# Optimization experiments

Hardware: AMD Instinct MI355X
Metric: run time of the kernel (lower is better)

The kernel has to match this reference:

```python
import jax, jax.numpy as jnp
import numpy as np

B, Lq, Lk = 2, 4096, 1024
Q_DIM, KV_DIM = 2048, 2048
H, HD = 16, 128          # n_heads, head_dim (nope part)
KVC, QC, R = 512, 768, 64  # kv_comp_dim, q_comp_dim, retr_dim (RoPE part)
LOOKBACK = 8
NEG = -1e30


def setup_inputs() -> dict:
    key = jax.random.key(0)
    ks = jax.random.split(key, 11)
    def w(k, shape, fan_in):
        return jax.random.normal(k, shape, jnp.float32) / np.sqrt(fan_in).astype(np.float32)
    return {
        'q': jax.random.normal(ks[0], (B, Lq, Q_DIM), jnp.float32),
        'kv': jax.random.normal(ks[1], (B, Lk, KV_DIM), jnp.float32),
        'seg_id': jnp.sort(jax.random.randint(ks[2], (B, Lq), 0, Lk), axis=-1),
        'W_kvc': w(ks[3], (KV_DIM, KVC), KV_DIM),   # kv_comp linear (no bias)
        'W_dq':  w(ks[4], (Q_DIM, QC), Q_DIM),      # query down-projection
        'W_uq':  w(ks[5], (QC, H * HD), QC),        # query up-proj (nope)
        'W_qr':  w(ks[6], (QC, H * R), QC),         # query rope proj
        'W_uk':  w(ks[7], (KVC, H * HD), KVC),      # key up-proj (nope)
        'W_kr':  w(ks[8], (KVC, R), KVC),           # shared key rope proj
        'W_uv':  w(ks[9], (KVC, H * HD), KVC),      # value up-proj
        'W_o':   w(ks[10], (H * HD, Q_DIM), H * HD),# output projection
    }


def _rope(x, L):
    # x: [..., L, R] with R even; positions 0..L-1 on the -2 axis.
    half = x.shape[-1] // 2
    inv_freq = 1.0 / (10000.0 ** (jnp.arange(half, dtype=jnp.float32) / half))
    ang = jnp.arange(L, dtype=jnp.float32)[:, None] * inv_freq  # [L, half]
    cos, sin = jnp.cos(ang), jnp.sin(ang)
    x1, x2 = x[..., :half], x[..., half:]
    return jnp.concatenate([x1 * cos - x2 * sin, x1 * sin + x2 * cos], axis=-1)


def reference(q, kv, seg_id, W_kvc, W_dq, W_uq, W_qr, W_uk, W_kr, W_uv, W_o):
    b, lq, _ = q.shape
    lk = kv.shape[1]
    kv_c = kv @ W_kvc                                   # [B,Lk,KVC]
    q_c = q @ W_dq                                      # [B,Lq,QC]
    q_nope = (q_c @ W_uq).reshape(b, lq, H, HD).transpose(0, 2, 1, 3)  # [B,H,Lq,HD]
    q_rope = (q_c @ W_qr).reshape(b, lq, H, R).transpose(0, 2, 1, 3)   # [B,H,Lq,R]
    k_nope = (kv_c @ W_uk).reshape(b, lk, H, HD)        # [B,Lk,H,HD]
    v = (kv_c @ W_uv).reshape(b, lk, H, HD)             # [B,Lk,H,HD]
    k_rope = kv_c @ W_kr                                # [B,Lk,R] shared across heads
    q_rope = _rope(q_rope, lq)
    k_rope = _rope(k_rope, lk)
    scale = 1.0 / np.sqrt(HD + R).astype(np.float32)
    scores = (jnp.einsum('bhqd,bkhd->bhqk', q_nope, k_nope)
              + jnp.einsum('bhqr,bkr->bhqk', q_rope, k_rope)) * scale
    # segment lookback block mask: allow q_seg - lookback <= k <= q_seg
    k_ids = jnp.arange(lk)[None, None, :]               # [1,1,Lk]
    qs = seg_id[:, :, None]                             # [B,Lq,1]
    good = (k_ids <= qs) & (k_ids >= qs - LOOKBACK)     # [B,Lq,Lk]
    scores = jnp.where(good[:, None, :, :], scores, NEG)
    attn = jax.nn.softmax(scores, axis=-1)              # [B,H,Lq,Lk]
    out = jnp.einsum('bhqk,bkhd->bqhd', attn, v).reshape(b, lq, H * HD)
    return out @ W_o                                    # [B,Lq,Q_DIM]
```

## Files before the change

### kernel.cpp

```cpp
#include <hip/hip_runtime.h>
#include <math.h>

typedef __bf16 bf16_t;
typedef __bf16 bf16x8 __attribute__((ext_vector_type(8)));
typedef float f32x4 __attribute__((ext_vector_type(4)));

#define B_    2
#define LQ    4096
#define LK    1024
#define QDIM  2048
#define KVDIM 2048
#define H_    16
#define HD_   128
#define KVC_  512
#define QC_   768
#define R_    64

#define QCOMB 3072
#define KCOMB 4224

typedef __attribute__((address_space(1))) void gvoid_t;
typedef __attribute__((address_space(3))) void lvoid_t;

static __device__ __forceinline__ void gld_lds16(const void* g, void* l) {
  __builtin_amdgcn_global_load_lds((gvoid_t*)(void*)g, (lvoid_t*)l, 16, 0, 0);
}

__global__ void cvt2_f32_bf16(const float* __restrict__ a, bf16_t* __restrict__ oa, long na,
                              const float* __restrict__ b, bf16_t* __restrict__ ob, long nb) {
  const long stride = (long)gridDim.x * blockDim.x * 8;
  for (long i = ((long)blockIdx.x * blockDim.x + threadIdx.x) * 8; i < na; i += stride) {
    float4 x = *(const float4*)(a + i);
    float4 y = *(const float4*)(a + i + 4);
    bf16x8 t;
    t[0] = (bf16_t)x.x; t[1] = (bf16_t)x.y; t[2] = (bf16_t)x.z; t[3] = (bf16_t)x.w;
    t[4] = (bf16_t)y.x; t[5] = (bf16_t)y.y; t[6] = (bf16_t)y.z; t[7] = (bf16_t)y.w;
    *(bf16x8*)(oa + i) = t;
  }
  for (long i = ((long)blockIdx.x * blockDim.x + threadIdx.x) * 8; i < nb; i += stride) {
    float4 x = *(const float4*)(b + i);
    float4 y = *(const float4*)(b + i + 4);
    bf16x8 t;
    t[0] = (bf16_t)x.x; t[1] = (bf16_t)x.y; t[2] = (bf16_t)x.z; t[3] = (bf16_t)x.w;
    t[4] = (bf16_t)y.x; t[5] = (bf16_t)y.y; t[6] = (bf16_t)y.z; t[7] = (bf16_t)y.w;
    *(bf16x8*)(ob + i) = t;
  }
}

struct TransAll {
  const float* src[8];
  bf16_t* dst[8];
  int K[8], N[8], gx[8];
  int off[9];
};

__global__ __launch_bounds__(256) void transpose_all(TransAll d) {
  const int bid = blockIdx.x;
  int i = 0;
#pragma unroll
  for (int j = 1; j < 8; ++j) if (bid >= d.off[j]) i = j;
  const float* __restrict__ src = d.src[i];
  bf16_t* __restrict__ dst = d.dst[i];
  const int K = d.K[i], N = d.N[i];
  const int local = bid - d.off[i];
  const int gx = d.gx[i];
  const int bx = (local % gx) * 32, by = (local / gx) * 32;
  __shared__ float t[32][33];
  const int x = threadIdx.x, y = threadIdx.y;
#pragma unroll
  for (int j = 0; j < 32; j += 8)
    t[y + j][x] = src[(size_t)(by + y + j) * N + bx + x];
  __syncthreads();
#pragma unroll
  for (int j = 0; j < 32; j += 8)
    dst[(size_t)(bx + y + j) * K + by + x] = (bf16_t)t[x][y + j];
}

template <typename CT>
__global__ __launch_bounds__(256) void gemm_bt(
    const bf16_t* __restrict__ A, const bf16_t* __restrict__ Bt,
    CT* __restrict__ C, int M, int N, int K) {
  __shared__ __align__(16) bf16_t lA[128 * 64];
  __shared__ __align__(16) bf16_t lB[128 * 64];
  const int tid = threadIdx.x;
  const int wave = tid >> 6, lane = tid & 63;

  const int gx = gridDim.x, gy = gridDim.y;
  const int nwg = gx * gy;
  int bx, by;
  if (((nwg & 7) == 0) && ((gy & 7) == 0)) {
    const int orig = blockIdx.y * gx + blockIdx.x;
    const int wg = (orig & 7) * (nwg >> 3) + (orig >> 3);
    const int gxB = gx << 3;
    const int band = wg / gxB, rem = wg % gxB;
    bx = rem >> 3;
    by = (band << 3) + (rem & 7);
  } else {
    bx = blockIdx.x; by = blockIdx.y;
  }

  const int row0 = by * 128, col0 = bx * 128;
  const int wr = (wave >> 1) * 64, wc = (wave & 1) * 64;
  f32x4 acc[4][4] = {};
  const int kT = K >> 6;
  const int lr = lane >> 3;
  const int lc8 = (lane & 7) * 8;

  for (int kt = 0; kt < kT; ++kt) {
    const int k0 = kt << 6;
    __syncthreads();
#pragma unroll
    for (int j = 0; j < 4; ++j) {
      const int c = wave * 4 + j;
      const bf16_t* ga = A + (size_t)(row0 + c * 8 + lr) * K + k0 + lc8;
      gld_lds16(ga, &lA[c * 512]);
      const bf16_t* gb = Bt + (size_t)(col0 + c * 8 + lr) * K + k0 + lc8;
      gld_lds16(gb, &lB[c * 512]);
    }
    __syncthreads();
#pragma unroll
    for (int kk = 0; kk < 2; ++kk) {
      bf16x8 af[4], bfr[4];
      const int kc = kk * 32 + (lane >> 4) * 8;
      const int fr = lane & 15;
#pragma unroll
      for (int m = 0; m < 4; ++m)
        af[m] = *(const bf16x8*)&lA[(wr + m * 16 + fr) * 64 + kc];
#pragma unroll
      for (int n = 0; n < 4; ++n)
        bfr[n] = *(const bf16x8*)&lB[(wc + n * 16 + fr) * 64 + kc];
#pragma unroll
      for (int m = 0; m < 4; ++m)
#pragma unroll
        for (int n = 0; n < 4; ++n)
          acc[m][n] = __builtin_amdgcn_mfma_f32_16x16x32_bf16(af[m], bfr[n], acc[m][n], 0, 0, 0);
    }
  }
  const int fr = lane & 15, fq = lane >> 4;
#pragma unroll
  for (int m = 0; m < 4; ++m)
#pragma unroll
    for (int n = 0; n < 4; ++n) {
      const int col = col0 + wc + n * 16 + fr;
#pragma unroll
      for (int r = 0; r < 4; ++r) {
        const int row = row0 + wr + m * 16 + fq * 4 + r;
        C[(size_t)row * N + col] = (CT)acc[m][n][r];
      }
    }
}

template <int TN, typename CT>
__global__ __launch_bounds__(512, 2) void gemm_big2(
    const bf16_t* __restrict__ A, const bf16_t* __restrict__ Bt,
    CT* __restrict__ C, int M, int N, int K) {
  constexpr int NF = TN / 64;
  constexpr int LW = 4 + TN / 64;
  __shared__ __align__(16) bf16_t lA[2][256 * 64];
  __shared__ __align__(16) bf16_t lB[2][TN * 64];
  const int tid = threadIdx.x;
  const int w = tid >> 6, lane = tid & 63;

  const int gx = gridDim.x;
  const int nwg = gx * gridDim.y;
  const int orig = blockIdx.y * gx + blockIdx.x;
  const int wg = (orig & 7) * (nwg >> 3) + (orig >> 3);
  const int bx = wg % gx, by = wg / gx;

  const int row0 = by * 256, col0 = bx * TN;
  const int wm = w >> 2, wn = w & 3;
  const int lr = lane >> 3;
  const int kswz = ((lane & 7) ^ lr) * 8;
  const int nt = K >> 6;
  const int fr = lane & 15, fq = lane >> 4;

  auto STAGE = [&](int t, int buf) {
    const int k0 = t << 6;
#pragma unroll
    for (int j = 0; j < 4; ++j) {
      const int s = j * 8 + w;
      gld_lds16(A + (size_t)(row0 + s * 8 + lr) * K + k0 + kswz, &lA[buf][s * 512]);
    }
#pragma unroll
    for (int j = 0; j < TN / 64; ++j) {
      const int s = j * 8 + w;
      gld_lds16(Bt + (size_t)(col0 + s * 8 + lr) * K + k0 + kswz, &lB[buf][s * 512]);
    }
  };

  bf16x8 aA[8], bA[NF], aB[8], bB[NF];
  f32x4 acc[8][NF];
#pragma unroll
  for (int i = 0; i < 8; ++i)
#pragma unroll
    for (int j = 0; j < NF; ++j) acc[i][j] = f32x4{0.f, 0.f, 0.f, 0.f};

  auto READ = [&](int buf, int kk, bf16x8* a, bf16x8* b) {
    const int swzk = (kk * 32 + fq * 8) ^ ((fr & 7) << 3);
#pragma unroll
    for (int mf = 0; mf < 8; ++mf)
      a[mf] = *(const bf16x8*)&lA[buf][(wm * 128 + mf * 16 + fr) * 64 + swzk];
#pragma unroll
    for (int nf = 0; nf < NF; ++nf)
      b[nf] = *(const bf16x8*)&lB[buf][(wn * (TN / 4) + nf * 16 + fr) * 64 + swzk];
  };
  auto MF = [&](bf16x8* a, bf16x8* b) {
    __builtin_amdgcn_s_setprio(1);
#pragma unroll
    for (int mf = 0; mf < 8; ++mf)
#pragma unroll
      for (int nf = 0; nf < NF; ++nf)
        acc[mf][nf] = __builtin_amdgcn_mfma_f32_16x16x32_bf16(a[mf], b[nf], acc[mf][nf], 0, 0, 0);
    __builtin_amdgcn_s_setprio(0);
  };

  STAGE(0, 0);
  STAGE(1, 1);
  if constexpr (LW == 8) { asm volatile("s_waitcnt vmcnt(8)" ::: "memory"); }
  else                   { asm volatile("s_waitcnt vmcnt(6)" ::: "memory"); }
  __builtin_amdgcn_sched_barrier(0);
  __builtin_amdgcn_s_barrier();
  READ(0, 0, aA, bA);

  for (int t = 0; t < nt; ++t) {
    const int buf = t & 1;
    READ(buf, 1, aB, bB);
    __builtin_amdgcn_sched_barrier(0);
    MF(aA, bA);
    asm volatile("s_waitcnt lgkmcnt(0)" ::: "memory");
    __builtin_amdgcn_sched_barrier(0);
    __builtin_amdgcn_s_barrier();
    if (t + 2 < nt) {
      STAGE(t + 2, buf);
      if constexpr (LW == 8) { asm volatile("s_waitcnt vmcnt(8)" ::: "memory"); }
      else                   { asm volatile("s_waitcnt vmcnt(6)" ::: "memory"); }
    } else {
      asm volatile("s_waitcnt vmcnt(0)" ::: "memory");
    }
    __builtin_amdgcn_sched_barrier(0);
    __builtin_amdgcn_s_barrier();
    if (t + 1 < nt) READ(buf ^ 1, 0, aA, bA);
    __builtin_amdgcn_sched_barrier(0);
    MF(aB, bB);
  }

#pragma unroll
  for (int mf = 0; mf < 8; ++mf)
#pragma unroll
    for (int nf = 0; nf < NF; ++nf) {
      const int col = col0 + wn * (TN / 4) + nf * 16 + fr;
#pragma unroll
      for (int r = 0; r < 4; ++r) {
        const int row = row0 + wm * 128 + mf * 16 + fq * 4 + r;
        C[(size_t)row * N + col] = (CT)acc[mf][nf][r];
      }
    }
}

#define SWZK_(ks) (((ks) * 32 + fq * 8) ^ ((fr & 7) << 3))
#define RD_A(buf, q) { _Pragma("unroll") for (int mf = 0; mf < 4; ++mf) { \
    ar[mf][0] = *(const bf16x8*)&lA[buf][wm][((q) * 64 + mf * 16 + fr) * 64 + SWZK_(0)]; \
    ar[mf][1] = *(const bf16x8*)&lA[buf][wm][((q) * 64 + mf * 16 + fr) * 64 + SWZK_(1)]; } }
#define RD_B(buf, nq) { _Pragma("unroll") for (int nf = 0; nf < 2; ++nf) { \
    br[nq][nf][0] = *(const bf16x8*)&lB[buf][wbh][(wbr + (nq) * 32 + nf * 16 + fr) * 64 + SWZK_(0)]; \
    br[nq][nf][1] = *(const bf16x8*)&lB[buf][wbh][(wbr + (nq) * 32 + nf * 16 + fr) * 64 + SWZK_(1)]; } }
#define MFMA_Q(mq, nq) { __builtin_amdgcn_s_setprio(1); \
  _Pragma("unroll") for (int mf = 0; mf < 4; ++mf) \
  _Pragma("unroll") for (int nf = 0; nf < 2; ++nf) { \
    acc[(mq)*4+mf][(nq)*2+nf] = __builtin_amdgcn_mfma_f32_16x16x32_bf16(ar[mf][0], br[nq][nf][0], acc[(mq)*4+mf][(nq)*2+nf], 0, 0, 0); \
    acc[(mq)*4+mf][(nq)*2+nf] = __builtin_amdgcn_mfma_f32_16x16x32_bf16(ar[mf][1], br[nq][nf][1], acc[(mq)*4+mf][(nq)*2+nf], 0, 0, 0); } \
  __builtin_amdgcn_s_setprio(0); }
#define SBAR_ __builtin_amdgcn_sched_barrier(0)
#define HBAR_ __builtin_amdgcn_s_barrier()
#define LGK0_ asm volatile("s_waitcnt lgkmcnt(0)" ::: "memory")

template <typename CT>
__global__ __launch_bounds__(512, 2) void gemm_8ph(
    const bf16_t* __restrict__ A, const bf16_t* __restrict__ Bt,
    CT* __restrict__ C, int M, int N, int K) {
  __shared__ __align__(16) bf16_t lA[2][2][128 * 64];
  __shared__ __align__(16) bf16_t lB[2][2][128 * 64];
  const int tid = threadIdx.x;
  const int w = tid >> 6, lane = tid & 63;

  const int gx = gridDim.x;
  const int nwg = gx * gridDim.y;
  const int orig = blockIdx.y * gx + blockIdx.x;
  const int wg = (orig & 7) * (nwg >> 3) + (orig >> 3);
  const int bx = wg % gx, by = wg / gx;

  const int row0 = by * 256, col0 = bx * 256;
  const int wm = w >> 2, wn = w & 3;
  const int lr = lane >> 3;
  const int kswz = ((lane & 7) ^ lr) * 8;
  const int nt = K >> 6;
  const int fr = lane & 15, fq = lane >> 4;
  const int wbh = wn >> 1;
  const int wbr = (wn & 1) * 64;

  auto stA = [&](int t, int h, int buf) {
    const bf16_t* g = A + (size_t)(row0 + h * 128 + w * 8 + lr) * K + (t << 6) + kswz;
    gld_lds16(g, &lA[buf][h][w * 8 * 64]);
    gld_lds16(g + (size_t)64 * K, &lA[buf][h][(64 + w * 8) * 64]);
  };
  auto stB = [&](int t, int h, int buf) {
    const bf16_t* g = Bt + (size_t)(col0 + h * 128 + w * 8 + lr) * K + (t << 6) + kswz;
    gld_lds16(g, &lB[buf][h][w * 8 * 64]);
    gld_lds16(g + (size_t)64 * K, &lB[buf][h][(64 + w * 8) * 64]);
  };

  bf16x8 ar[4][2], br[2][2][2];
  f32x4 acc[8][4];
#pragma unroll
  for (int i = 0; i < 8; ++i)
#pragma unroll
    for (int j = 0; j < 4; ++j) acc[i][j] = f32x4{0.f, 0.f, 0.f, 0.f};

  stA(0, 0, 0); stA(0, 1, 0); stB(0, 0, 0); stB(0, 1, 0);
  stB(1, 0, 1); stB(1, 1, 1);
  asm volatile("s_waitcnt vmcnt(4)" ::: "memory");
  SBAR_; HBAR_;

  for (int t = 0; t < nt; ++t) {
    const int buf = t & 1;
    SBAR_;
    RD_A(buf, 0); RD_B(buf, 0);
    if (t + 1 < nt) stA(t + 1, 0, buf ^ 1);
    SBAR_; HBAR_; LGK0_; SBAR_;
    MFMA_Q(0, 0);
    SBAR_; HBAR_;
    SBAR_;
    RD_B(buf, 1);
    if (t + 1 < nt) stA(t + 1, 1, buf ^ 1);
    SBAR_; HBAR_; LGK0_; SBAR_;
    MFMA_Q(0, 1);
    SBAR_; HBAR_;
    SBAR_;
    RD_A(buf, 1);
    if (t + 2 < nt) stB(t + 2, 0, buf);
    SBAR_; HBAR_; LGK0_; SBAR_;
    MFMA_Q(1, 1);
    SBAR_; HBAR_;
    SBAR_;
    if (t + 2 < nt) {
      stB(t + 2, 1, buf);
      asm volatile("s_waitcnt vmcnt(4)" ::: "memory");
    } else {
      asm volatile("s_waitcnt vmcnt(0)" ::: "memory");
    }
    SBAR_; HBAR_; SBAR_;
    MFMA_Q(1, 0);
    SBAR_; HBAR_;
  }

#pragma unroll
  for (int mfg = 0; mfg < 8; ++mfg)
#pragma unroll
    for (int nfg = 0; nfg < 4; ++nfg) {
      const int col = col0 + wn * 64 + (nfg >> 1) * 32 + (nfg & 1) * 16 + fr;
#pragma unroll
      for (int r = 0; r < 4; ++r) {
        const int row = row0 + wm * 128 + mfg * 16 + fq * 4 + r;
        C[(size_t)row * N + col] = (CT)acc[mfg][nfg][r];
      }
    }
}

#define QROPE_BLOCKS ((B_ * LQ * H_) / 8)
__global__ __launch_bounds__(256) void rope2_kernel(bf16_t* __restrict__ qbase, bf16_t* __restrict__ kvbase) {
  const int bid = blockIdx.x;
  bf16_t* base;
  int tokStride, hshift, posMask;
  long bidl;
  if (bid < QROPE_BLOCKS) { base = qbase; tokStride = QCOMB; hshift = 4; posMask = LQ - 1; bidl = bid; }
  else { base = kvbase; tokStride = KCOMB; hshift = 0; posMask = LK - 1; bidl = bid - QROPE_BLOCKS; }
  const long idx = bidl * 8 + (threadIdx.x >> 5);
  const int i = threadIdx.x & 31;
  const long tok = idx >> hshift;
  const int h = (int)(idx & ((1 << hshift) - 1));
  const int pos = (int)(tok & posMask);
  bf16_t* p = base + tok * (long)tokStride + h * 64;
  const float x1 = (float)p[i], x2 = (float)p[i + 32];
  const float invf = expf(-((float)i * (1.0f / 32.f)) * 9.210340371976184f);
  float sn, cs;
  sincosf((float)pos * invf, &sn, &cs);
  p[i]      = (bf16_t)(x1 * cs - x2 * sn);
  p[i + 32] = (bf16_t)(x1 * sn + x2 * cs);
}

__global__ __launch_bounds__(256) void attn_sparse(
    const bf16_t* __restrict__ qc, const bf16_t* __restrict__ kvc,
    const int* __restrict__ seg, bf16_t* __restrict__ out) {
  const int qrow = blockIdx.x * 4 + (threadIdx.x >> 6);
  const int lane = threadIdx.x & 63;
  const int h = lane >> 2, sub = lane & 3;
  const int b = qrow >> 12;
  const int s = seg[qrow];
  const int kl = max(0, s - 8);
  const float scale = 0.07216878364870322f;

  float qnf[32], qrf[16];
  {
    const bf16_t* p = qc + (size_t)qrow * QCOMB + h * HD_ + sub * 32;
#pragma unroll
    for (int j = 0; j < 4; ++j) {
      bf16x8 t = *(const bf16x8*)(p + j * 8);
#pragma unroll
      for (int e = 0; e < 8; ++e) qnf[j * 8 + e] = (float)t[e];
    }
    const bf16_t* p2 = qc + (size_t)qrow * QCOMB + 2048 + h * R_ + sub * 16;
#pragma unroll
    for (int j = 0; j < 2; ++j) {
      bf16x8 t = *(const bf16x8*)(p2 + j * 8);
#pragma unroll
      for (int e = 0; e < 8; ++e) qrf[j * 8 + e] = (float)t[e];
    }
  }

  float sc[9];
#pragma unroll
  for (int kk = 0; kk < 9; ++kk) {
    const int kx = kl + kk;
    const bf16_t* kb = kvc + (size_t)(b * LK + kx) * KCOMB;
    float d = 0.f;
    const bf16_t* p = kb + h * HD_ + sub * 32;
#pragma unroll
    for (int j = 0; j < 4; ++j) {
      bf16x8 t = *(const bf16x8*)(p + j * 8);
#pragma unroll
      for (int e = 0; e < 8; ++e) d += qnf[j * 8 + e] * (float)t[e];
    }
    const bf16_t* p2 = kb + 4096 + sub * 16;
#pragma unroll
    for (int j = 0; j < 2; ++j) {
      bf16x8 t = *(const bf16x8*)(p2 + j * 8);
#pragma unroll
      for (int e = 0; e < 8; ++e) d += qrf[j * 8 + e] * (float)t[e];
    }
    d += __shfl_xor(d, 1);
    d += __shfl_xor(d, 2);
    sc[kk] = (kx <= s) ? d * scale : -1e30f;
  }
  float m = sc[0];
#pragma unroll
  for (int kk = 1; kk < 9; ++kk) m = fmaxf(m, sc[kk]);
  float sum = 0.f;
#pragma unroll
  for (int kk = 0; kk < 9; ++kk) { const float p = expf(sc[kk] - m); sc[kk] = p; sum += p; }
  const float inv = 1.f / sum;

  float o[32];
#pragma unroll
  for (int j = 0; j < 32; ++j) o[j] = 0.f;
#pragma unroll
  for (int kk = 0; kk < 9; ++kk) {
    const bf16_t* pv = kvc + (size_t)(b * LK + kl + kk) * KCOMB + 2048 + h * HD_ + sub * 32;
    const float p = sc[kk] * inv;
#pragma unroll
    for (int j = 0; j < 4; ++j) {
      bf16x8 t = *(const bf16x8*)(pv + j * 8);
#pragma unroll
      for (int e = 0; e < 8; ++e) o[j * 8 + e] += p * (float)t[e];
    }
  }
  bf16_t* po = out + (size_t)qrow * (H_ * HD_) + h * HD_ + sub * 32;
#pragma unroll
  for (int j = 0; j < 4; ++j) {
    bf16x8 t;
#pragma unroll
    for (int e = 0; e < 8; ++e) t[e] = (bf16_t)o[j * 8 + e];
    *(bf16x8*)(po + j * 8) = t;
  }
}

extern "C" void kernel_launch(void* const* d_in, const int* in_sizes, int n_in,
                              void* d_out, int out_size, void* d_ws, size_t ws_size,
                              hipStream_t stream) {
  const float* q     = (const float*)d_in[0];
  const float* kv    = (const float*)d_in[1];
  const int*   seg   = (const int*)d_in[2];
  const float* W_kvc = (const float*)d_in[3];
  const float* W_dq  = (const float*)d_in[4];
  const float* W_uq  = (const float*)d_in[5];
  const float* W_qr  = (const float*)d_in[6];
  const float* W_uk  = (const float*)d_in[7];
  const float* W_kr  = (const float*)d_in[8];
  const float* W_uv  = (const float*)d_in[9];
  const float* W_o   = (const float*)d_in[10];
  float* out = (float*)d_out;
  (void)in_sizes; (void)n_in; (void)out_size; (void)ws_size;

  char* ws = (char*)d_ws;
  size_t off = 0;
  auto alloc = [&](size_t bytes) {
    char* p = ws + off;
    off = (off + bytes + 255) & ~(size_t)255;
    return p;
  };
  bf16_t* q_bf    = (bf16_t*)alloc((size_t)B_ * LQ * QDIM * 2);
  bf16_t* kv_bf   = (bf16_t*)alloc((size_t)B_ * LK * KVDIM * 2);
  bf16_t* WkvcT   = (bf16_t*)alloc((size_t)KVC_ * KVDIM * 2);
  bf16_t* WdqT    = (bf16_t*)alloc((size_t)QC_ * QDIM * 2);
  bf16_t* WuqrT   = (bf16_t*)alloc((size_t)QCOMB * QC_ * 2);
  bf16_t* WkvT    = (bf16_t*)alloc((size_t)KCOMB * KVC_ * 2);
  bf16_t* WoT     = (bf16_t*)alloc((size_t)QDIM * (H_ * HD_) * 2);
  bf16_t* kv_c    = (bf16_t*)alloc((size_t)B_ * LK * KVC_ * 2);
  bf16_t* q_c     = (bf16_t*)alloc((size_t)B_ * LQ * QC_ * 2);
  bf16_t* q_comb  = (bf16_t*)alloc((size_t)B_ * LQ * QCOMB * 2);
  bf16_t* kv_comb = (bf16_t*)alloc((size_t)B_ * LK * KCOMB * 2);
  bf16_t* attn_o  = q_bf;

  cvt2_f32_bf16<<<4096, 256, 0, stream>>>(q, q_bf, (long)B_ * LQ * QDIM,
                                          kv, kv_bf, (long)B_ * LK * KVDIM);

  {
    TransAll d;
    auto set = [&](int i, const float* s, bf16_t* dt, int K, int N) {
      d.src[i] = s; d.dst[i] = dt; d.K[i] = K; d.N[i] = N; d.gx[i] = N / 32;
    };
    set(0, W_kvc, WkvcT, KVDIM, KVC_);
    set(1, W_dq,  WdqT,  QDIM,  QC_);
    set(2, W_uq,  WuqrT, QC_,   H_ * HD_);
    set(3, W_qr,  WuqrT + (size_t)(H_ * HD_) * QC_, QC_, H_ * R_);
    set(4, W_uk,  WkvT,  KVC_,  H_ * HD_);
    set(5, W_uv,  WkvT + (size_t)(H_ * HD_) * KVC_, KVC_, H_ * HD_);
    set(6, W_kr,  WkvT + (size_t)2 * (H_ * HD_) * KVC_, KVC_, R_);
    set(7, W_o,   WoT,   H_ * HD_, QDIM);
    int acc_off = 0;
    for (int i = 0; i < 8; ++i) {
      d.off[i] = acc_off;
      acc_off += (d.N[i] / 32) * (d.K[i] / 32);
    }
    d.off[8] = acc_off;
    transpose_all<<<acc_off, dim3(32, 8), 0, stream>>>(d);
  }

  gemm_bt<bf16_t><<<dim3(KVC_ / 128, (B_ * LK) / 128), 256, 0, stream>>>(
      kv_bf, WkvcT, kv_c, B_ * LK, KVC_, KVDIM);
  gemm_big2<128, bf16_t><<<dim3(QC_ / 128, (B_ * LQ) / 256), 512, 0, stream>>>(
      q_bf, WdqT, q_c, B_ * LQ, QC_, QDIM);
  gemm_8ph<bf16_t><<<dim3(QCOMB / 256, (B_ * LQ) / 256), 512, 0, stream>>>(
      q_c, WuqrT, q_comb, B_ * LQ, QCOMB, QC_);
  gemm_big2<128, bf16_t><<<dim3(KCOMB / 128, (B_ * LK) / 256), 512, 0, stream>>>(
      kv_c, WkvT, kv_comb, B_ * LK, KCOMB, KVC_);

  rope2_kernel<<<QROPE_BLOCKS + (B_ * LK) / 8, 256, 0, stream>>>(q_comb + 2048, kv_comb + 4096);

  attn_sparse<<<(B_ * LQ) / 4, 256, 0, stream>>>(q_comb, kv_comb, seg, attn_o);

  gemm_8ph<float><<<dim3(QDIM / 256, (B_ * LQ) / 256), 512, 0, stream>>>(
      attn_o, WoT, out, B_ * LQ, QDIM, H_ * HD_);
}
```

Baseline: 338.5 us.

## Software-pipeline LDS fragment reads across MFMA phases in 8-phase GEMM

Restructures the GEMM main loop so that the LDS reads for the next MFMA quadrant, including the first quadrant of the next K tile, are issued before the current quadrant's MFMAs. The explicit lgkmcnt(0) waits are removed and the loop is unrolled by two with ping-pong B register buffers. The aim is to hide LDS read latency behind matrix math instead of stalling before each phase. It raises VGPR pressure under 512x2 launch bounds and assumes nt is even.

```diff
diff --git a/kernel.cpp b/kernel.cpp
--- a/kernel.cpp
+++ b/kernel.cpp
@@ -258,21 +258,46 @@
 }
 
 #define SWZK_(ks) (((ks) * 32 + fq * 8) ^ ((fr & 7) << 3))
-#define RD_A(buf, q) { _Pragma("unroll") for (int mf = 0; mf < 4; ++mf) { \
-    ar[mf][0] = *(const bf16x8*)&lA[buf][wm][((q) * 64 + mf * 16 + fr) * 64 + SWZK_(0)]; \
-    ar[mf][1] = *(const bf16x8*)&lA[buf][wm][((q) * 64 + mf * 16 + fr) * 64 + SWZK_(1)]; } }
-#define RD_B(buf, nq) { _Pragma("unroll") for (int nf = 0; nf < 2; ++nf) { \
-    br[nq][nf][0] = *(const bf16x8*)&lB[buf][wbh][(wbr + (nq) * 32 + nf * 16 + fr) * 64 + SWZK_(0)]; \
-    br[nq][nf][1] = *(const bf16x8*)&lB[buf][wbh][(wbr + (nq) * 32 + nf * 16 + fr) * 64 + SWZK_(1)]; } }
-#define MFMA_Q(mq, nq) { __builtin_amdgcn_s_setprio(1); \
+#define RDA(buf, q, dst) { _Pragma("unroll") for (int mf = 0; mf < 4; ++mf) { \
+    dst[mf][0] = *(const bf16x8*)&lA[buf][wm][((q) * 64 + mf * 16 + fr) * 64 + SWZK_(0)]; \
+    dst[mf][1] = *(const bf16x8*)&lA[buf][wm][((q) * 64 + mf * 16 + fr) * 64 + SWZK_(1)]; } }
+#define RDB(buf, nq, dst) { _Pragma("unroll") for (int nf = 0; nf < 2; ++nf) { \
+    dst[nf][0] = *(const bf16x8*)&lB[buf][wbh][(wbr + (nq) * 32 + nf * 16 + fr) * 64 + SWZK_(0)]; \
+    dst[nf][1] = *(const bf16x8*)&lB[buf][wbh][(wbr + (nq) * 32 + nf * 16 + fr) * 64 + SWZK_(1)]; } }
+#define MFQ(a, b, mq, nq) { __builtin_amdgcn_s_setprio(1); \
   _Pragma("unroll") for (int mf = 0; mf < 4; ++mf) \
   _Pragma("unroll") for (int nf = 0; nf < 2; ++nf) { \
-    acc[(mq)*4+mf][(nq)*2+nf] = __builtin_amdgcn_mfma_f32_16x16x32_bf16(ar[mf][0], br[nq][nf][0], acc[(mq)*4+mf][(nq)*2+nf], 0, 0, 0); \
-    acc[(mq)*4+mf][(nq)*2+nf] = __builtin_amdgcn_mfma_f32_16x16x32_bf16(ar[mf][1], br[nq][nf][1], acc[(mq)*4+mf][(nq)*2+nf], 0, 0, 0); } \
+    acc[(mq)*4+mf][(nq)*2+nf] = __builtin_amdgcn_mfma_f32_16x16x32_bf16(a[mf][0], b[nf][0], acc[(mq)*4+mf][(nq)*2+nf], 0, 0, 0); \
+    acc[(mq)*4+mf][(nq)*2+nf] = __builtin_amdgcn_mfma_f32_16x16x32_bf16(a[mf][1], b[nf][1], acc[(mq)*4+mf][(nq)*2+nf], 0, 0, 0); } \
   __builtin_amdgcn_s_setprio(0); }
 #define SBAR_ __builtin_amdgcn_sched_barrier(0)
 #define HBAR_ __builtin_amdgcn_s_barrier()
-#define LGK0_ asm volatile("s_waitcnt lgkmcnt(0)" ::: "memory")
+
+#define TILE8(t, B0C, B0N) { \
+  const int buf = (t) & 1; \
+   \
+  if ((t) + 1 < nt) stA((t) + 1, 0, buf ^ 1); \
+  RDB(buf, 1, br1); \
+  SBAR_; MFQ(arC, B0C, 0, 0); SBAR_; HBAR_; \
+   \
+  if ((t) + 1 < nt) stA((t) + 1, 1, buf ^ 1); \
+  RDA(buf, 1, arN); \
+  SBAR_; MFQ(arC, br1, 0, 1); SBAR_; HBAR_; \
+   \
+  if ((t) + 2 < nt) stB((t) + 2, 0, buf); \
+  if ((t) + 1 < nt) { \
+    asm volatile("s_waitcnt vmcnt(6)" ::: "memory"); \
+    SBAR_; HBAR_; SBAR_; \
+    RDB(buf ^ 1, 0, B0N); \
+  } \
+  SBAR_; MFQ(arN, br1, 1, 1); SBAR_; HBAR_; \
+   \
+  if ((t) + 2 < nt) { stB((t) + 2, 1, buf); asm volatile("s_waitcnt vmcnt(4)" ::: "memory"); } \
+  else { asm volatile("s_waitcnt vmcnt(0)" ::: "memory"); } \
+  SBAR_; HBAR_; SBAR_; \
+  if ((t) + 1 < nt) RDA(buf ^ 1, 0, arC); \
+  SBAR_; MFQ(arN, B0C, 1, 0); SBAR_; HBAR_; \
+}
 
 template <typename CT>
 __global__ __launch_bounds__(512, 2) void gemm_8ph(
@@ -309,7 +334,7 @@
     gld_lds16(g + (size_t)64 * K, &lB[buf][h][(64 + w * 8) * 64]);
   };
 
-  bf16x8 ar[4][2], br[2][2][2];
+  bf16x8 arC[4][2], arN[4][2], br1[2][2], brE[2][2], brO[2][2];
   f32x4 acc[8][4];
 #pragma unroll
   for (int i = 0; i < 8; ++i)
@@ -319,38 +344,13 @@
   stA(0, 0, 0); stA(0, 1, 0); stB(0, 0, 0); stB(0, 1, 0);
   stB(1, 0, 1); stB(1, 1, 1);
   asm volatile("s_waitcnt vmcnt(4)" ::: "memory");
-  SBAR_; HBAR_;
-
-  for (int t = 0; t < nt; ++t) {
-    const int buf = t & 1;
-    SBAR_;
-    RD_A(buf, 0); RD_B(buf, 0);
-    if (t + 1 < nt) stA(t + 1, 0, buf ^ 1);
-    SBAR_; HBAR_; LGK0_; SBAR_;
-    MFMA_Q(0, 0);
-    SBAR_; HBAR_;
-    SBAR_;
-    RD_B(buf, 1);
-    if (t + 1 < nt) stA(t + 1, 1, buf ^ 1);
-    SBAR_; HBAR_; LGK0_; SBAR_;
-    MFMA_Q(0, 1);
-    SBAR_; HBAR_;
-    SBAR_;
-    RD_A(buf, 1);
-    if (t + 2 < nt) stB(t + 2, 0, buf);
-    SBAR_; HBAR_; LGK0_; SBAR_;
-    MFMA_Q(1, 1);
-    SBAR_; HBAR_;
-    SBAR_;
-    if (t + 2 < nt) {
-      stB(t + 2, 1, buf);
-      asm volatile("s_waitcnt vmcnt(4)" ::: "memory");
-    } else {
-      asm volatile("s_waitcnt vmcnt(0)" ::: "memory");
-    }
-    SBAR_; HBAR_; SBAR_;
-    MFMA_Q(1, 0);
-    SBAR_; HBAR_;
+  SBAR_; HBAR_; SBAR_;
+  RDA(0, 0, arC); RDB(0, 0, brE);
+  SBAR_;
+
+  for (int t = 0; t < nt; t += 2) {
+    TILE8(t, brE, brO);
+    TILE8(t + 1, brO, brE);
   }
 
 #pragma unroll
```

Result: slower. 391.8 us (+15.8%).
